# Performance work log

Hardware: AMD Instinct MI355X
Metric: run time of the kernel (lower is better)

Reference implementation:

```python
import jax, jax.numpy as jnp
import numpy as np

T, D, E, K = 8192, 4096, 64, 8


def setup_inputs() -> dict:
    key = jax.random.key(0)
    k1, k2, k3, k4 = jax.random.split(key, 4)
    x = jax.random.normal(k1, (T, D), dtype=jnp.float32)
    # nn.Linear stores weight as [out_features, in_features]
    Wg = jax.random.normal(k2, (E, D), dtype=jnp.float32) * (1.0 / np.sqrt(D))
    Wc = jax.random.normal(k3, (E, D), dtype=jnp.float32) * (1.0 / np.sqrt(D))
    extra_scale = jnp.zeros((E,), dtype=jnp.float32)  # init zeros as in module
    extra_bias = jax.random.normal(k4, (E,), dtype=jnp.float32) * 0.01
    return {"x": x, "Wg": Wg, "Wc": Wc, "extra_scale": extra_scale,
            "extra_bias": extra_bias, "topk": K}


def reference(x, Wg, Wc, extra_scale, extra_bias, topk):
    # scores = |classifier(x) * silu(gate(x))|, softmax in fp32
    gate = jnp.einsum('td,ed->te', x, Wg)        # [T, E]
    cls = jnp.einsum('td,ed->te', x, Wc)         # [T, E]
    scores = jnp.abs(cls * jax.nn.silu(gate))
    scores = jax.nn.softmax(scores.astype(jnp.float32), axis=-1)
    biased = scores + extra_bias[None, :]        # load-balance bias, used only for selection
    _, indices = jax.lax.top_k(biased, topk)     # [T, K]
    original = 1.0 + scores * extra_scale[None, :]
    weights = jnp.take_along_axis(original, indices, axis=1)  # [T, K]
    return weights.astype(x.dtype), indices
```

## Files before the change

### kernel.cpp

```cpp
#include <hip/hip_runtime.h>
#include <math.h>


#define T_DIM 8192
#define D_DIM 4096
#define E_DIM 64
#define N2    128
#define MB    128
#define BK    32
#define LDA   132
#define KTOP  8

__global__ __launch_bounds__(256, 2)
void router_gemm(const float* __restrict__ x,
                 const float* __restrict__ Wg,
                 const float* __restrict__ Wc,
                 float* __restrict__ P,
                 int sliceK)
{
    __shared__ float sx[BK][LDA];
    __shared__ float sw[BK][LDA];

    const int tid = threadIdx.x;
    const int mb  = blockIdx.x;
    const int ks  = blockIdx.y;

    const int r2 = tid >> 1;
    const int kq = tid & 1;

    const int k0 = ks * sliceK;

    const float4* xp = (const float4*)(x + (size_t)(mb * MB + r2) * D_DIM + k0 + kq * 16);
    const float*  wrow = (r2 < E_DIM) ? (Wg + (size_t)r2 * D_DIM)
                                      : (Wc + (size_t)(r2 - E_DIM) * D_DIM);
    const float4* wp = (const float4*)(wrow + k0 + kq * 16);

    float4 rx[4], rw[4];
    #pragma unroll
    for (int q = 0; q < 4; ++q) { rx[q] = xp[q]; rw[q] = wp[q]; }

    float acc[8][8];
    #pragma unroll
    for (int i = 0; i < 8; ++i)
        #pragma unroll
        for (int j = 0; j < 8; ++j) acc[i][j] = 0.f;

    const int tm8 = (tid & 15) * 8;
    const int tn8 = (tid >> 4) * 8;
    const int NS  = sliceK / BK;

    for (int s = 0; s < NS; ++s) {
        #pragma unroll
        for (int q = 0; q < 4; ++q) {
            const int k = kq * 16 + q * 4;
            sx[k+0][r2] = rx[q].x; sx[k+1][r2] = rx[q].y;
            sx[k+2][r2] = rx[q].z; sx[k+3][r2] = rx[q].w;
            sw[k+0][r2] = rw[q].x; sw[k+1][r2] = rw[q].y;
            sw[k+2][r2] = rw[q].z; sw[k+3][r2] = rw[q].w;
        }
        __syncthreads();

        if (s + 1 < NS) {
            xp += 8; wp += 8;
            #pragma unroll
            for (int q = 0; q < 4; ++q) { rx[q] = xp[q]; rw[q] = wp[q]; }
        }

        #pragma unroll
        for (int kk = 0; kk < BK; ++kk) {
            const float4 a0 = *(const float4*)&sx[kk][tm8];
            const float4 a1 = *(const float4*)&sx[kk][tm8 + 4];
            const float4 b0 = *(const float4*)&sw[kk][tn8];
            const float4 b1 = *(const float4*)&sw[kk][tn8 + 4];
            const float a[8] = {a0.x,a0.y,a0.z,a0.w,a1.x,a1.y,a1.z,a1.w};
            const float b[8] = {b0.x,b0.y,b0.z,b0.w,b1.x,b1.y,b1.z,b1.w};
            #pragma unroll
            for (int i = 0; i < 8; ++i)
                #pragma unroll
                for (int j = 0; j < 8; ++j)
                    acc[i][j] = fmaf(a[i], b[j], acc[i][j]);
        }
        __syncthreads();
    }

    float* Pr = P + ((size_t)ks * T_DIM + (size_t)mb * MB + tm8) * N2 + tn8;
    #pragma unroll
    for (int i = 0; i < 8; ++i) {
        const float4 s0 = make_float4(acc[i][0], acc[i][1], acc[i][2], acc[i][3]);
        const float4 s1 = make_float4(acc[i][4], acc[i][5], acc[i][6], acc[i][7]);
        *(float4*)&Pr[(size_t)i * N2]     = s0;
        *(float4*)&Pr[(size_t)i * N2 + 4] = s1;
    }
}

__global__ __launch_bounds__(256)
void router_topk(const float* __restrict__ P,
                 const float* __restrict__ scale,
                 const float* __restrict__ bias,
                 float* __restrict__ out,
                 int ksplit)
{
    const int lane = threadIdx.x & 63;
    const int wid  = threadIdx.x >> 6;
    const int row  = blockIdx.x * 4 + wid;

    float g = 0.f, c = 0.f;
    for (int ks = 0; ks < ksplit; ++ks) {
        const float* p = P + ((size_t)ks * T_DIM + row) * N2;
        g += p[lane];
        c += p[E_DIM + lane];
    }
    const float sg = g / (1.f + expf(-g));
    const float v  = fabsf(c * sg);

    float m = v;
    #pragma unroll
    for (int off = 32; off >= 1; off >>= 1) m = fmaxf(m, __shfl_xor(m, off));
    const float e = expf(v - m);
    float Z = e;
    #pragma unroll
    for (int off = 32; off >= 1; off >>= 1) Z += __shfl_xor(Z, off);
    const float s = e / Z;

    const float sc  = scale[lane];
    float cur = s + bias[lane];

    float myw = 0.f; int myi = 0;
    #pragma unroll
    for (int j = 0; j < KTOP; ++j) {
        float bv = cur; int bi = lane;
        #pragma unroll
        for (int off = 32; off >= 1; off >>= 1) {
            const float ov = __shfl_xor(bv, off);
            const int   oi = __shfl_xor(bi, off);
            if (ov > bv || (ov == bv && oi < bi)) { bv = ov; bi = oi; }
        }
        const float s_bi  = __shfl(s,  bi);
        const float sc_bi = __shfl(sc, bi);
        const float w = 1.f + s_bi * sc_bi;
        if (lane == j)  { myw = w; myi = bi; }
        if (lane == bi) cur = -INFINITY;
    }

    if (lane < KTOP) {
        out[(size_t)row * KTOP + lane] = myw;
        out[(size_t)T_DIM * KTOP + (size_t)row * KTOP + lane] = (float)myi;
    }
}

extern "C" void kernel_launch(void* const* d_in, const int* in_sizes, int n_in,
                              void* d_out, int out_size, void* d_ws, size_t ws_size,
                              hipStream_t stream)
{
    const float* x  = (const float*)d_in[0];
    const float* Wg = (const float*)d_in[1];
    const float* Wc = (const float*)d_in[2];
    const float* sc = (const float*)d_in[3];
    const float* bs = (const float*)d_in[4];
    float* out = (float*)d_out;
    float* P   = (float*)d_ws;

    int ksplit = 8;
    const size_t per = (size_t)T_DIM * N2 * sizeof(float);
    while (ksplit > 1 && (size_t)ksplit * per > ws_size) ksplit >>= 1;
    const int sliceK = D_DIM / ksplit;

    dim3 g1(T_DIM / MB, ksplit);
    router_gemm<<<g1, 256, 0, stream>>>(x, Wg, Wc, P, sliceK);
    router_topk<<<T_DIM / 4, 256, 0, stream>>>(P, sc, bs, out, ksplit);
}
```

Measured before the change: 278.6 us.

## Replace FP32 SIMT GEMM with 3-way bf16-split MFMA emulation

The scalar-FMA shared-memory GEMM is replaced by MFMA 32x32x16 bf16 instructions, with each fp32 value split into hi/mid/lo bf16 parts and six cross-product MFMAs per tile to keep near-fp32 accuracy. A new prep kernel pre-splits the router weights into three bf16 arrays in the workspace every call. The x tiles are split on the fly in registers, and B fragments are read directly from global memory without LDS staging. This trades extra MFMA work and uncached weight loads for much higher matrix throughput, and top-k selection could flip on near-ties if accuracy falls short.

```diff
diff --git a/kernel.cpp b/kernel.cpp
--- a/kernel.cpp
+++ b/kernel.cpp
@@ -6,91 +6,133 @@
 #define D_DIM 4096
 #define E_DIM 64
 #define N2    128
-#define MB    128
-#define BK    32
-#define LDA   132
 #define KTOP  8
+#define MB_ROWS 128
+
+typedef __attribute__((ext_vector_type(8)))  short bfrag8;
+typedef __attribute__((ext_vector_type(16))) float f32x16;
+
+__device__ __forceinline__ unsigned short f2bf_rne(float f) {
+    unsigned int u = __float_as_uint(f);
+    unsigned int r = u + 0x7fffu + ((u >> 16) & 1u);
+    return (unsigned short)(r >> 16);
+}
+__device__ __forceinline__ float bf2f(unsigned short h) {
+    return __uint_as_float(((unsigned int)h) << 16);
+}
+__device__ __forceinline__ void split3(float v, unsigned short& h,
+                                       unsigned short& m, unsigned short& l) {
+    h = f2bf_rne(v);
+    const float r1 = v - bf2f(h);
+    m = f2bf_rne(r1);
+    const float r2 = r1 - bf2f(m);
+    l = f2bf_rne(r2);
+}
+
+__global__ __launch_bounds__(256)
+void router_prep(const float* __restrict__ Wg, const float* __restrict__ Wc,
+                 unsigned short* __restrict__ Whi, unsigned short* __restrict__ Wmid,
+                 unsigned short* __restrict__ Wlo)
+{
+    const int i   = blockIdx.x * 256 + threadIdx.x;
+    const int row = i >> 10;
+    const float* src = (row < E_DIM) ? (Wg + (size_t)row * D_DIM)
+                                     : (Wc + (size_t)(row - E_DIM) * D_DIM);
+    const float4 w = ((const float4*)src)[i & 1023];
+    const float v[4] = {w.x, w.y, w.z, w.w};
+    ushort4 hv, mv, lv;
+    split3(v[0], hv.x, mv.x, lv.x);
+    split3(v[1], hv.y, mv.y, lv.y);
+    split3(v[2], hv.z, mv.z, lv.z);
+    split3(v[3], hv.w, mv.w, lv.w);
+    *(ushort4*)(Whi  + (size_t)i * 4) = hv;
+    *(ushort4*)(Wmid + (size_t)i * 4) = mv;
+    *(ushort4*)(Wlo  + (size_t)i * 4) = lv;
+}
 
 __global__ __launch_bounds__(256, 2)
 void router_gemm(const float* __restrict__ x,
-                 const float* __restrict__ Wg,
-                 const float* __restrict__ Wc,
+                 const unsigned short* __restrict__ Whi,
+                 const unsigned short* __restrict__ Wmid,
+                 const unsigned short* __restrict__ Wlo,
                  float* __restrict__ P,
                  int sliceK)
 {
-    __shared__ float sx[BK][LDA];
-    __shared__ float sw[BK][LDA];
-
-    const int tid = threadIdx.x;
-    const int mb  = blockIdx.x;
-    const int ks  = blockIdx.y;
-
-    const int r2 = tid >> 1;
-    const int kq = tid & 1;
-
-    const int k0 = ks * sliceK;
-
-    const float4* xp = (const float4*)(x + (size_t)(mb * MB + r2) * D_DIM + k0 + kq * 16);
-    const float*  wrow = (r2 < E_DIM) ? (Wg + (size_t)r2 * D_DIM)
-                                      : (Wc + (size_t)(r2 - E_DIM) * D_DIM);
-    const float4* wp = (const float4*)(wrow + k0 + kq * 16);
-
-    float4 rx[4], rw[4];
-    #pragma unroll
-    for (int q = 0; q < 4; ++q) { rx[q] = xp[q]; rw[q] = wp[q]; }
-
-    float acc[8][8];
-    #pragma unroll
-    for (int i = 0; i < 8; ++i)
-        #pragma unroll
-        for (int j = 0; j < 8; ++j) acc[i][j] = 0.f;
-
-    const int tm8 = (tid & 15) * 8;
-    const int tn8 = (tid >> 4) * 8;
-    const int NS  = sliceK / BK;
-
-    for (int s = 0; s < NS; ++s) {
-        #pragma unroll
-        for (int q = 0; q < 4; ++q) {
-            const int k = kq * 16 + q * 4;
-            sx[k+0][r2] = rx[q].x; sx[k+1][r2] = rx[q].y;
-            sx[k+2][r2] = rx[q].z; sx[k+3][r2] = rx[q].w;
-            sw[k+0][r2] = rw[q].x; sw[k+1][r2] = rw[q].y;
-            sw[k+2][r2] = rw[q].z; sw[k+3][r2] = rw[q].w;
-        }
-        __syncthreads();
-
-        if (s + 1 < NS) {
-            xp += 8; wp += 8;
+    const int tid  = threadIdx.x;
+    const int lane = tid & 63;
+    const int wid  = tid >> 6;
+    const int l31  = lane & 31;
+    const int lh   = lane >> 5;
+    const int mb   = blockIdx.x;
+    const int ks   = blockIdx.y;
+    const int k0   = ks * sliceK;
+    const int kend = k0 + sliceK;
+    const int row0 = mb * MB_ROWS + wid * 32;
+
+    f32x16 acc[4];
+    #pragma unroll
+    for (int n = 0; n < 4; ++n)
+        #pragma unroll
+        for (int r = 0; r < 16; ++r)
+            acc[n][r] = 0.f;
+
+    const float* xr = x + (size_t)(row0 + l31) * D_DIM;
+
+    const float* xp0 = xr + k0 + lh * 8;
+    float4 a00 = *(const float4*)(xp0);
+    float4 a01 = *(const float4*)(xp0 + 4);
+    float4 a10 = *(const float4*)(xp0 + 16);
+    float4 a11 = *(const float4*)(xp0 + 20);
+
+    for (int kk = k0; kk < kend; kk += 32) {
+        bfrag8 ah[2], am[2], al[2];
+        {
+            const float av0[8] = {a00.x,a00.y,a00.z,a00.w,a01.x,a01.y,a01.z,a01.w};
+            const float av1[8] = {a10.x,a10.y,a10.z,a10.w,a11.x,a11.y,a11.z,a11.w};
             #pragma unroll
-            for (int q = 0; q < 4; ++q) { rx[q] = xp[q]; rw[q] = wp[q]; }
-        }
-
-        #pragma unroll
-        for (int kk = 0; kk < BK; ++kk) {
-            const float4 a0 = *(const float4*)&sx[kk][tm8];
-            const float4 a1 = *(const float4*)&sx[kk][tm8 + 4];
-            const float4 b0 = *(const float4*)&sw[kk][tn8];
-            const float4 b1 = *(const float4*)&sw[kk][tn8 + 4];
-            const float a[8] = {a0.x,a0.y,a0.z,a0.w,a1.x,a1.y,a1.z,a1.w};
-            const float b[8] = {b0.x,b0.y,b0.z,b0.w,b1.x,b1.y,b1.z,b1.w};
+            for (int j = 0; j < 8; ++j) {
+                unsigned short h, m, l;
+                split3(av0[j], h, m, l);
+                ah[0][j] = (short)h; am[0][j] = (short)m; al[0][j] = (short)l;
+                split3(av1[j], h, m, l);
+                ah[1][j] = (short)h; am[1][j] = (short)m; al[1][j] = (short)l;
+            }
+        }
+
+        if (kk + 32 < kend) {
+            const float* xp = xr + (kk + 32) + lh * 8;
+            a00 = *(const float4*)(xp);
+            a01 = *(const float4*)(xp + 4);
+            a10 = *(const float4*)(xp + 16);
+            a11 = *(const float4*)(xp + 20);
+        }
+
+        #pragma unroll
+        for (int n = 0; n < 4; ++n) {
             #pragma unroll
-            for (int i = 0; i < 8; ++i)
-                #pragma unroll
-                for (int j = 0; j < 8; ++j)
-                    acc[i][j] = fmaf(a[i], b[j], acc[i][j]);
-        }
-        __syncthreads();
-    }
-
-    float* Pr = P + ((size_t)ks * T_DIM + (size_t)mb * MB + tm8) * N2 + tn8;
-    #pragma unroll
-    for (int i = 0; i < 8; ++i) {
-        const float4 s0 = make_float4(acc[i][0], acc[i][1], acc[i][2], acc[i][3]);
-        const float4 s1 = make_float4(acc[i][4], acc[i][5], acc[i][6], acc[i][7]);
-        *(float4*)&Pr[(size_t)i * N2]     = s0;
-        *(float4*)&Pr[(size_t)i * N2 + 4] = s1;
-    }
+            for (int h2 = 0; h2 < 2; ++h2) {
+                const size_t bo = (size_t)(n * 32 + l31) * D_DIM + kk + h2 * 16 + lh * 8;
+                const bfrag8 bh = *(const bfrag8*)(Whi  + bo);
+                const bfrag8 bm = *(const bfrag8*)(Wmid + bo);
+                const bfrag8 bl = *(const bfrag8*)(Wlo  + bo);
+                acc[n] = __builtin_amdgcn_mfma_f32_32x32x16_bf16(ah[h2], bl, acc[n], 0, 0, 0);
+                acc[n] = __builtin_amdgcn_mfma_f32_32x32x16_bf16(al[h2], bh, acc[n], 0, 0, 0);
+                acc[n] = __builtin_amdgcn_mfma_f32_32x32x16_bf16(am[h2], bm, acc[n], 0, 0, 0);
+                acc[n] = __builtin_amdgcn_mfma_f32_32x32x16_bf16(ah[h2], bm, acc[n], 0, 0, 0);
+                acc[n] = __builtin_amdgcn_mfma_f32_32x32x16_bf16(am[h2], bh, acc[n], 0, 0, 0);
+                acc[n] = __builtin_amdgcn_mfma_f32_32x32x16_bf16(ah[h2], bh, acc[n], 0, 0, 0);
+            }
+        }
+    }
+
+    float* Pb = P + ((size_t)ks * T_DIM + row0) * N2 + l31;
+    #pragma unroll
+    for (int n = 0; n < 4; ++n)
+        #pragma unroll
+        for (int r = 0; r < 16; ++r) {
+            const int wrow = (r & 3) + 8 * (r >> 2) + 4 * lh;
+            Pb[(size_t)wrow * N2 + n * 32] = acc[n][r];
+        }
 }
 
 __global__ __launch_bounds__(256)
@@ -160,12 +202,18 @@
     float* out = (float*)d_out;
     float* P   = (float*)d_ws;
 
-    int ksplit = 8;
-    const size_t per = (size_t)T_DIM * N2 * sizeof(float);
-    while (ksplit > 1 && (size_t)ksplit * per > ws_size) ksplit >>= 1;
-    const int sliceK = D_DIM / ksplit;
-
-    dim3 g1(T_DIM / MB, ksplit);
-    router_gemm<<<g1, 256, 0, stream>>>(x, Wg, Wc, P, sliceK);
-    router_topk<<<T_DIM / 4, 256, 0, stream>>>(P, sc, bs, out, ksplit);
-}
+    const size_t PER = (size_t)T_DIM * N2 * sizeof(float);
+    const size_t WSP = (size_t)N2 * D_DIM * sizeof(unsigned short);
+
+    int S = 8;
+    while (S > 1 && (size_t)S * PER + 3 * WSP > ws_size) S >>= 1;
+    const int sliceK = D_DIM / S;
+
+    unsigned short* Whi  = (unsigned short*)((char*)d_ws + (size_t)S * PER);
+    unsigned short* Wmid = Whi + (size_t)N2 * D_DIM;
+    unsigned short* Wlo  = Wmid + (size_t)N2 * D_DIM;
+
+    router_prep<<<512, 256, 0, stream>>>(Wg, Wc, Whi, Wmid, Wlo);
+    router_gemm<<<dim3(T_DIM / MB_ROWS, S), 256, 0, stream>>>(x, Whi, Wmid, Wlo, P, sliceK);
+    router_topk<<<T_DIM / 4, 256, 0, stream>>>(P, sc, bs, out, S);
+}
```

After: 303.7 us. 9.0% more time.
